# Optimization experiments

Measured on AMD Instinct MI355X. Metric: run time of the kernel, lower is better.

The kernel has to match this reference:

```python
import jax, jax.numpy as jnp
import numpy as np

N = 100_000   # total nodes across all subgraphs in batch
E = 1_600_000 # edges (avg degree 16)
B = 1_000     # number of subgraphs
D = 128       # in_dim = out_dim
SZ = N // B   # nodes per subgraph


def setup_inputs() -> dict:
    key = jax.random.key(0)
    ks = jax.random.split(key, 8)
    feat = jax.random.normal(ks[0], (N, D), dtype=jnp.float32)
    edge_src = jax.random.randint(ks[1], (E,), 0, N, dtype=jnp.int32)
    edge_dst = jax.random.randint(ks[2], (E,), 0, N, dtype=jnp.int32)
    # pre-normalized edge weights (is_normed=True path)
    edge_w = jax.random.uniform(ks[3], (E,), dtype=jnp.float32)
    s = 1.0 / np.sqrt(D)
    W1 = jax.random.normal(ks[4], (D, D), dtype=jnp.float32) * s
    W2 = jax.random.normal(ks[5], (D, D), dtype=jnp.float32) * s
    Wp = jax.random.normal(ks[6], (D, D), dtype=jnp.float32) * s
    b1 = jnp.zeros((D,), jnp.float32)
    b2 = jnp.zeros((D,), jnp.float32)
    bp = jnp.zeros((D,), jnp.float32)
    # contiguous equal-size subgraphs; target = first node of each subgraph
    seg_ids = jnp.repeat(jnp.arange(B, dtype=jnp.int32), SZ)
    target = jnp.arange(B, dtype=jnp.int32) * SZ
    size_subg = jnp.full((B,), float(SZ), jnp.float32)
    return dict(feat=feat, edge_w=edge_w, W1=W1, b1=b1, W2=W2, b2=b2,
                Wp=Wp, bp=bp, size_subg=size_subg,
                edge_src=edge_src, edge_dst=edge_dst,
                seg_ids=seg_ids, target=target)


def _gcn_layer(x, src, dst, w, W, b):
    # sparse A_hat @ x : gather src features, weight, scatter-add into dst
    msg = x[src] * w[:, None]                       # [E, D]
    agg = jax.ops.segment_sum(msg, dst, num_segments=N)  # [N, D]
    return jax.nn.relu(agg @ W + b)


def reference(feat, edge_w, W1, b1, W2, b2, Wp, bp, size_subg,
              edge_src, edge_dst, seg_ids, target):
    # two stacked GCN layers (self.structure = [structure1, structure2])
    h1 = _gcn_layer(feat, edge_src, edge_dst, edge_w, W1, b1)
    h2 = _gcn_layer(h1, edge_src, edge_dst, edge_w, W2, b2)
    # ResPool: residual-sum over layer outputs, mean pool per subgraph,
    # add target-node embedding (residual), then linear + relu
    h = h1 + h2                                              # [N, D]
    pooled = jax.ops.segment_sum(h, seg_ids, num_segments=B)
    pooled = pooled / size_subg[:, None] + h[target]         # [B, D]
    emb = jax.nn.relu(pooled @ Wp + bp)
    # F.normalize(p=2, dim=1), eps=1e-12
    norm = jnp.sqrt(jnp.sum(emb * emb, axis=1, keepdims=True))
    emb = emb / jnp.maximum(norm, 1e-12)
    return emb  # EnsembleDummy just returns the single branch
```

## Files before the change

### kernel.cpp

```cpp
#include <hip/hip_runtime.h>

#define DD 128
#define CHUNK 4096
#define BSH 8
#define MAXBK 512
#define MAXCH 512
#define CAP 6144
#define CAPN 48
#define SLDS 4608

typedef _Float16 half8 __attribute__((ext_vector_type(8)));
typedef _Float16 half4v __attribute__((ext_vector_type(4)));
typedef float floatx4 __attribute__((ext_vector_type(4)));
typedef float floatx2 __attribute__((ext_vector_type(2)));

__global__ __launch_bounds__(512) void k_hist(const int* __restrict__ dst,
                                              int* __restrict__ histT, int E) {
    __shared__ int lhist[MAXBK];
    int tid = threadIdx.x;
    lhist[tid] = 0;
    __syncthreads();
    int beg = blockIdx.x * CHUNK;
    int end = min(beg + CHUNK, E);
    for (int k = beg + tid; k < end; k += 512)
        atomicAdd(&lhist[dst[k] >> BSH], 1);
    __syncthreads();
    histT[tid * MAXCH + blockIdx.x] = lhist[tid];
}

__global__ __launch_bounds__(512) void k_scanprep(int* __restrict__ histT,
                                                  int* __restrict__ gcur, int nChunks,
                                                  int NB,
                                                  const float* __restrict__ W1,
                                                  _Float16* __restrict__ W1t,
                                                  const float* __restrict__ W2,
                                                  _Float16* __restrict__ W2t) {
    if (blockIdx.x < NB) {
        __shared__ int wsum[8];
        int b = blockIdx.x;
        int c = threadIdx.x;
        int v = (c < nChunks) ? histT[b * MAXCH + c] : 0;
        int lane = c & 63, wave = c >> 6;
        int inc = v;
        #pragma unroll
        for (int off = 1; off < 64; off <<= 1) {
            int t = __shfl_up(inc, off, 64);
            if (lane >= off) inc += t;
        }
        if (lane == 63) wsum[wave] = inc;
        __syncthreads();
        if (c == 0) {
            int run = 0;
            #pragma unroll
            for (int j = 0; j < 8; ++j) { int t = wsum[j]; wsum[j] = run; run += t; }
        }
        __syncthreads();
        int ex = inc - v + wsum[wave];
        if (c < nChunks) histT[b * MAXCH + c] = ex;
        if (c == nChunks - 1) gcur[b] = ex + v;
    } else {
        int idx = (blockIdx.x - NB) * 512 + threadIdx.x;
        if (idx < 2 * DD * DD) {
            const float* W = (idx < DD * DD) ? W1 : W2;
            _Float16* Wt = (idx < DD * DD) ? W1t : W2t;
            int id = idx & (DD * DD - 1);
            int n = id >> 7, k = id & 127;
            Wt[n * DD + k] = (_Float16)W[k * DD + n];
        }
    }
}

__global__ __launch_bounds__(512) void k_pass1(const int* __restrict__ src,
                                               const int* __restrict__ dst,
                                               const float* __restrict__ w,
                                               const int* __restrict__ histT,
                                               int2* __restrict__ out, int E, int NB) {
    __shared__ int2 stg[CHUNK];
    __shared__ unsigned short bok[CHUNK];
    __shared__ int lhist[MAXBK];
    __shared__ int loff[MAXBK];
    __shared__ int lbase[MAXBK];
    __shared__ int lcur[MAXBK];
    int tid = threadIdx.x;
    lhist[tid] = 0;
    __syncthreads();

    int beg = blockIdx.x * CHUNK;
    int end = min(beg + CHUNK, E);
    for (int k = beg + tid; k < end; k += 512)
        atomicAdd(&lhist[dst[k] >> BSH], 1);
    __syncthreads();
    if (tid < 64) {
        int base = tid * 8, v[8], s = 0;
        #pragma unroll
        for (int j = 0; j < 8; ++j) { v[j] = lhist[base + j]; s += v[j]; }
        int scn = s;
        #pragma unroll
        for (int off = 1; off < 64; off <<= 1) {
            int t = __shfl_up(scn, off, 64);
            if (tid >= off) scn += t;
        }
        int ex = scn - s;
        #pragma unroll
        for (int j = 0; j < 8; ++j) { loff[base + j] = ex; lcur[base + j] = ex; ex += v[j]; }
    }
    __syncthreads();
    if (tid < NB)
        lbase[tid] = tid * CAP + histT[tid * MAXCH + blockIdx.x];
    for (int k = beg + tid; k < end; k += 512) {
        int d = dst[k];
        int b = d >> BSH;
        int p = atomicAdd(&lcur[b], 1);
        stg[p] = make_int2(src[k] | ((d & ((1 << BSH) - 1)) << 17),
                           __float_as_int(w[k]));
        bok[p] = (unsigned short)b;
    }
    __syncthreads();
    int total = end - beg;
    for (int j = tid; j < total; j += 512) {
        int b = bok[j];
        out[lbase[b] + (j - loff[b])] = stg[j];
    }
}

__global__ __launch_bounds__(512) void k_p2g1(const int2* __restrict__ bkt,
                                              const int* __restrict__ gcur,
                                              int* __restrict__ cnt,
                                              int2* __restrict__ edges, int N, int NB,
                                              const float* __restrict__ A,
                                              const _Float16* __restrict__ Wt,
                                              unsigned char* __restrict__ Y, int nrows) {
    if (blockIdx.x < NB) {
        __shared__ int2 stg[SLDS];
        __shared__ int lhist[1 << BSH];
        __shared__ int loff[1 << BSH];
        __shared__ int lcur[1 << BSH];
        int tid = threadIdx.x;
        int b = blockIdx.x;
        int base = b * CAP;
        int nrec = gcur[b];
        int nl = min(nrec, SLDS);
        int d0 = b << BSH;

        if (tid < (1 << BSH)) lhist[tid] = 0;
        for (int i = tid; i < nl; i += 512)
            stg[i] = bkt[base + i];
        __syncthreads();
        for (int i = tid; i < nl; i += 512)
            atomicAdd(&lhist[(unsigned)stg[i].x >> 17], 1);
        for (int i = SLDS + tid; i < nrec; i += 512)
            atomicAdd(&lhist[(unsigned)bkt[base + i].x >> 17], 1);
        __syncthreads();
        if (tid < 64) {
            int bs = tid * 4, vv[4], s = 0;
            #pragma unroll
            for (int j = 0; j < 4; ++j) { vv[j] = lhist[bs + j]; s += vv[j]; }
            int scn = s;
            #pragma unroll
            for (int off = 1; off < 64; off <<= 1) {
                int t = __shfl_up(scn, off, 64);
                if (tid >= off) scn += t;
            }
            int ex = scn - s;
            #pragma unroll
            for (int j = 0; j < 4; ++j) {
                loff[bs + j] = ex; lcur[bs + j] = ex; ex += vv[j];
            }
        }
        __syncthreads();
        if (tid < (1 << BSH)) {
            int d = d0 + tid;
            if (d < N)
                cnt[d] = min(lhist[tid], CAPN);
        }
        for (int i = tid; i < nl; i += 512) {
            int2 r = stg[i];
            int dl = (unsigned)r.x >> 17;
            int slot = atomicAdd(&lcur[dl], 1) - loff[dl];
            if (slot < CAPN)
                edges[(size_t)(d0 + dl) * CAPN + slot] = make_int2(r.x & 0x1FFFF, r.y);
        }
        for (int i = SLDS + tid; i < nrec; i += 512) {
            int2 r = bkt[base + i];
            int dl = (unsigned)r.x >> 17;
            int slot = atomicAdd(&lcur[dl], 1) - loff[dl];
            if (slot < CAPN)
                edges[(size_t)(d0 + dl) * CAPN + slot] = make_int2(r.x & 0x1FFFF, r.y);
        }
    } else {
        int gblk = blockIdx.x - NB;
        int wave = threadIdx.x >> 6;
        int lane = threadIdx.x & 63;
        int row0 = gblk * 256 + wave * 32;
        int m = lane & 15;
        int q = lane >> 4;
        int r0 = min(row0 + m, nrows - 1);
        int r1 = min(row0 + 16 + m, nrows - 1);

        floatx4 acc[2][8];
        #pragma unroll
        for (int t = 0; t < 2; ++t)
            #pragma unroll
            for (int c = 0; c < 8; ++c)
                acc[t][c] = (floatx4){0.f, 0.f, 0.f, 0.f};

        #pragma unroll
        for (int ks = 0; ks < 4; ++ks) {
            int kbase = ks * 32 + q * 8;
            float4 x0 = *reinterpret_cast<const float4*>(A + (size_t)r0 * DD + kbase);
            float4 x1 = *reinterpret_cast<const float4*>(A + (size_t)r0 * DD + kbase + 4);
            float4 y0 = *reinterpret_cast<const float4*>(A + (size_t)r1 * DD + kbase);
            float4 y1 = *reinterpret_cast<const float4*>(A + (size_t)r1 * DD + kbase + 4);
            half8 a0, a1;
            a0[0]=(_Float16)x0.x; a0[1]=(_Float16)x0.y; a0[2]=(_Float16)x0.z; a0[3]=(_Float16)x0.w;
            a0[4]=(_Float16)x1.x; a0[5]=(_Float16)x1.y; a0[6]=(_Float16)x1.z; a0[7]=(_Float16)x1.w;
            a1[0]=(_Float16)y0.x; a1[1]=(_Float16)y0.y; a1[2]=(_Float16)y0.z; a1[3]=(_Float16)y0.w;
            a1[4]=(_Float16)y1.x; a1[5]=(_Float16)y1.y; a1[6]=(_Float16)y1.z; a1[7]=(_Float16)y1.w;
            #pragma unroll
            for (int c = 0; c < 8; ++c) {
                half8 b = *reinterpret_cast<const half8*>(Wt + (size_t)(c * 16 + m) * DD + kbase);
                acc[0][c] = __builtin_amdgcn_mfma_f32_16x16x32_f16(b, a0, acc[0][c], 0, 0, 0);
                acc[1][c] = __builtin_amdgcn_mfma_f32_16x16x32_f16(b, a1, acc[1][c], 0, 0, 0);
            }
        }

        #pragma unroll
        for (int t = 0; t < 2; ++t) {
            int row = row0 + t * 16 + m;
            if (row >= nrows) continue;
            size_t rb = (size_t)row * DD;
            #pragma unroll
            for (int c = 0; c < 8; ++c) {
                int col = c * 16 + q * 4;
                int u = 0;
                u = __builtin_amdgcn_cvt_pk_fp8_f32(acc[t][c][0], acc[t][c][1], u, false);
                u = __builtin_amdgcn_cvt_pk_fp8_f32(acc[t][c][2], acc[t][c][3], u, true);
                *reinterpret_cast<unsigned int*>(&Y[rb + col]) = (unsigned int)u;
            }
        }
    }
}

__global__ __launch_bounds__(256) void k_gemm_f16A(const _Float16* __restrict__ A,
                                                   const _Float16* __restrict__ Wt,
                                                   unsigned char* __restrict__ Y,
                                                   int nrows) {
    int wave = threadIdx.x >> 6;
    int lane = threadIdx.x & 63;
    int row0 = blockIdx.x * 128 + wave * 32;
    int m = lane & 15;
    int q = lane >> 4;

    floatx4 acc[2][8];
    #pragma unroll
    for (int t = 0; t < 2; ++t)
        #pragma unroll
        for (int c = 0; c < 8; ++c)
            acc[t][c] = (floatx4){0.f, 0.f, 0.f, 0.f};

    #pragma unroll
    for (int ks = 0; ks < 4; ++ks) {
        int kbase = ks * 32 + q * 8;
        half8 a0 = *reinterpret_cast<const half8*>(A + (size_t)(row0 + m) * DD + kbase);
        half8 a1 = *reinterpret_cast<const half8*>(A + (size_t)(row0 + 16 + m) * DD + kbase);
        #pragma unroll
        for (int c = 0; c < 8; ++c) {
            half8 b = *reinterpret_cast<const half8*>(Wt + (size_t)(c * 16 + m) * DD + kbase);
            acc[0][c] = __builtin_amdgcn_mfma_f32_16x16x32_f16(b, a0, acc[0][c], 0, 0, 0);
            acc[1][c] = __builtin_amdgcn_mfma_f32_16x16x32_f16(b, a1, acc[1][c], 0, 0, 0);
        }
    }

    #pragma unroll
    for (int t = 0; t < 2; ++t) {
        int row = row0 + t * 16 + m;
        if (row >= nrows) continue;
        size_t rb = (size_t)row * DD;
        #pragma unroll
        for (int c = 0; c < 8; ++c) {
            int col = c * 16 + q * 4;
            int u = 0;
            u = __builtin_amdgcn_cvt_pk_fp8_f32(acc[t][c][0], acc[t][c][1], u, false);
            u = __builtin_amdgcn_cvt_pk_fp8_f32(acc[t][c][2], acc[t][c][3], u, true);
            *reinterpret_cast<unsigned int*>(&Y[rb + col]) = (unsigned int)u;
        }
    }
}

__global__ __launch_bounds__(256) void k_agg_eplg(const unsigned char* __restrict__ x,
                                                  const int* __restrict__ cnt,
                                                  const int2* __restrict__ edges,
                                                  const float* __restrict__ bias,
                                                  const _Float16* __restrict__ resid,
                                                  _Float16* __restrict__ out, int N) {
    int gwave = (blockIdx.x * blockDim.x + threadIdx.x) >> 6;
    int lane = threadIdx.x & 63;
    int half = lane >> 5;
    int hl = lane & 31;
    int wid = gwave * 2 + half;
    if (wid >= N) return;
    int g = hl >> 3;
    int sl = hl & 7;
    int c = cnt[wid];
    int beg = wid * CAPN;
    floatx2 acc2[8];
    #pragma unroll
    for (int j = 0; j < 8; ++j) acc2[j] = (floatx2){0.f, 0.f};

    int2 e[8];
    #pragma unroll
    for (int u = 0; u < 8; ++u) e[u] = edges[beg + u * 4 + g];
    uint4 v[8];
    #pragma unroll
    for (int u = 0; u < 8; ++u) {
        int row = min(max(e[u].x, 0), N - 1);
        v[u] = *reinterpret_cast<const uint4*>(x + (size_t)row * DD + sl * 16);
    }
    int end = min(c, CAPN);
    #pragma unroll
    for (int u = 0; u < 8; ++u) {
        float wv = (u * 4 + g < end) ? __int_as_float(e[u].y) : 0.f;
        floatx2 w2 = (floatx2){wv, wv};
        acc2[0] += __builtin_amdgcn_cvt_pk_f32_fp8((int)v[u].x, false) * w2;
        acc2[1] += __builtin_amdgcn_cvt_pk_f32_fp8((int)v[u].x, true)  * w2;
        acc2[2] += __builtin_amdgcn_cvt_pk_f32_fp8((int)v[u].y, false) * w2;
        acc2[3] += __builtin_amdgcn_cvt_pk_f32_fp8((int)v[u].y, true)  * w2;
        acc2[4] += __builtin_amdgcn_cvt_pk_f32_fp8((int)v[u].z, false) * w2;
        acc2[5] += __builtin_amdgcn_cvt_pk_f32_fp8((int)v[u].z, true)  * w2;
        acc2[6] += __builtin_amdgcn_cvt_pk_f32_fp8((int)v[u].w, false) * w2;
        acc2[7] += __builtin_amdgcn_cvt_pk_f32_fp8((int)v[u].w, true)  * w2;
    }
    if (end > 32) {
        int2 e2[4];
        #pragma unroll
        for (int u = 0; u < 4; ++u) e2[u] = edges[beg + 32 + u * 4 + g];
        uint4 v2[4];
        #pragma unroll
        for (int u = 0; u < 4; ++u) {
            int row = min(max(e2[u].x, 0), N - 1);
            v2[u] = *reinterpret_cast<const uint4*>(x + (size_t)row * DD + sl * 16);
        }
        #pragma unroll
        for (int u = 0; u < 4; ++u) {
            float wv = (32 + u * 4 + g < end) ? __int_as_float(e2[u].y) : 0.f;
            floatx2 w2 = (floatx2){wv, wv};
            acc2[0] += __builtin_amdgcn_cvt_pk_f32_fp8((int)v2[u].x, false) * w2;
            acc2[1] += __builtin_amdgcn_cvt_pk_f32_fp8((int)v2[u].x, true)  * w2;
            acc2[2] += __builtin_amdgcn_cvt_pk_f32_fp8((int)v2[u].y, false) * w2;
            acc2[3] += __builtin_amdgcn_cvt_pk_f32_fp8((int)v2[u].y, true)  * w2;
            acc2[4] += __builtin_amdgcn_cvt_pk_f32_fp8((int)v2[u].z, false) * w2;
            acc2[5] += __builtin_amdgcn_cvt_pk_f32_fp8((int)v2[u].z, true)  * w2;
            acc2[6] += __builtin_amdgcn_cvt_pk_f32_fp8((int)v2[u].w, false) * w2;
            acc2[7] += __builtin_amdgcn_cvt_pk_f32_fp8((int)v2[u].w, true)  * w2;
        }
    }

    #pragma unroll
    for (int j = 0; j < 8; ++j) {
        acc2[j][0] += __shfl_xor(acc2[j][0], 8, 64);
        acc2[j][1] += __shfl_xor(acc2[j][1], 8, 64);
        acc2[j][0] += __shfl_xor(acc2[j][0], 16, 64);
        acc2[j][1] += __shfl_xor(acc2[j][1], 16, 64);
    }
    if (g == 0) {
        float acc[16];
        #pragma unroll
        for (int j = 0; j < 8; ++j) { acc[2 * j] = acc2[j][0]; acc[2 * j + 1] = acc2[j][1]; }
        size_t rb = (size_t)wid * DD + sl * 16;
        float bb[16];
        #pragma unroll
        for (int q = 0; q < 4; ++q) {
            float4 b4 = *reinterpret_cast<const float4*>(&bias[sl * 16 + q * 4]);
            bb[q * 4 + 0] = b4.x; bb[q * 4 + 1] = b4.y;
            bb[q * 4 + 2] = b4.z; bb[q * 4 + 3] = b4.w;
        }
        half8 o0, o1;
        if (resid) {
            half8 r0 = *reinterpret_cast<const half8*>(&resid[rb]);
            half8 r1 = *reinterpret_cast<const half8*>(&resid[rb + 8]);
            #pragma unroll
            for (int j = 0; j < 8; ++j) {
                float v = acc[j] + bb[j];
                v = v > 0.f ? v : 0.f;
                o0[j] = (_Float16)(v + (float)r0[j]);
            }
            #pragma unroll
            for (int j = 0; j < 8; ++j) {
                float v = acc[8 + j] + bb[8 + j];
                v = v > 0.f ? v : 0.f;
                o1[j] = (_Float16)(v + (float)r1[j]);
            }
        } else {
            #pragma unroll
            for (int j = 0; j < 8; ++j) {
                float v = acc[j] + bb[j];
                o0[j] = (_Float16)(v > 0.f ? v : 0.f);
            }
            #pragma unroll
            for (int j = 0; j < 8; ++j) {
                float v = acc[8 + j] + bb[8 + j];
                o1[j] = (_Float16)(v > 0.f ? v : 0.f);
            }
        }
        *reinterpret_cast<half8*>(&out[rb]) = o0;
        *reinterpret_cast<half8*>(&out[rb + 8]) = o1;
    }
}

__global__ __launch_bounds__(256) void k_pool_final(const _Float16* __restrict__ h,
                                                    const int* __restrict__ target,
                                                    const float* __restrict__ size_subg,
                                                    const float* __restrict__ Wp,
                                                    const float* __restrict__ bp,
                                                    float* __restrict__ out, int SZ) {
    __shared__ float part[16][DD];
    __shared__ float p[DD];
    __shared__ float wsum[2];
    int b = blockIdx.x;
    int t = threadIdx.x;
    int c = t & 15;
    int r = t >> 4;
    const _Float16* hp = h + (size_t)b * SZ * DD;
    float s[8] = {0.f, 0.f, 0.f, 0.f, 0.f, 0.f, 0.f, 0.f};
    for (int n = r; n < SZ; n += 16) {
        half8 v = *reinterpret_cast<const half8*>(hp + (size_t)n * DD + c * 8);
        #pragma unroll
        for (int j = 0; j < 8; ++j) s[j] += (float)v[j];
    }
    #pragma unroll
    for (int j = 0; j < 8; ++j) part[r][c * 8 + j] = s[j];
    __syncthreads();
    if (t < DD) {
        float sum = 0.f;
        #pragma unroll
        for (int rr = 0; rr < 16; ++rr) sum += part[rr][t];
        int tg = target[b];
        p[t] = sum / size_subg[b] + (float)h[(size_t)tg * DD + t];
    }
    __syncthreads();
    if (t < DD) {
        float acc = 0.f;
        #pragma unroll 4
        for (int k = 0; k < DD; ++k) acc = fmaf(p[k], Wp[k * DD + t], acc);
        float e = acc + bp[t];
        e = e > 0.f ? e : 0.f;
        float sq = e * e;
        #pragma unroll
        for (int off = 32; off > 0; off >>= 1) sq += __shfl_down(sq, off, 64);
        int lane = t & 63, w = t >> 6;
        if (lane == 0) wsum[w] = sq;
        __syncthreads();
        float norm = sqrtf(wsum[0] + wsum[1]);
        float scale = 1.f / fmaxf(norm, 1e-12f);
        out[b * DD + t] = e * scale;
    } else {
        __syncthreads();
    }
}

extern "C" void kernel_launch(void* const* d_in, const int* in_sizes, int n_in,
                              void* d_out, int out_size, void* d_ws, size_t ws_size,
                              hipStream_t stream) {
    const float* feat      = (const float*)d_in[0];
    const float* edge_w    = (const float*)d_in[1];
    const float* W1        = (const float*)d_in[2];
    const float* b1        = (const float*)d_in[3];
    const float* W2        = (const float*)d_in[4];
    const float* b2        = (const float*)d_in[5];
    const float* Wp        = (const float*)d_in[6];
    const float* bp        = (const float*)d_in[7];
    const float* size_subg = (const float*)d_in[8];
    const int*   edge_src  = (const int*)d_in[9];
    const int*   edge_dst  = (const int*)d_in[10];
    const int*   target    = (const int*)d_in[12];

    const int N  = in_sizes[0] / DD;
    const int E  = in_sizes[1];
    const int B  = in_sizes[8];
    const int SZ = N / B;

    const int P  = ((N + 127) / 128) * 128;
    const int NB = (N + (1 << BSH) - 1) >> BSH;
    const int nChunks = (E + CHUNK - 1) / CHUNK;

    char* ws = (char*)d_ws;
    size_t off = 0;
    auto alloc = [&](size_t bytes) {
        void* p = ws + off;
        off += (bytes + 255) & ~(size_t)255;
        return p;
    };
    unsigned char* Y = (unsigned char*)alloc((size_t)P * DD);
    _Float16* h1     = (_Float16*)alloc((size_t)P * DD * 2);
    _Float16* H      = (_Float16*)alloc((size_t)P * DD * 2);
    _Float16* W1t    = (_Float16*)alloc((size_t)DD * DD * 2);
    _Float16* W2t    = (_Float16*)alloc((size_t)DD * DD * 2);
    int*   cnt       = (int*)alloc((size_t)N * 4);
    int*   gcur      = (int*)alloc((size_t)MAXBK * 4);
    int*   histT     = (int*)alloc((size_t)MAXBK * MAXCH * 4);
    int2*  edges_bkt = (int2*)alloc((size_t)NB * CAP * 8);
    int2*  edges     = (int2*)alloc((size_t)N * CAPN * 8);

    k_hist<<<nChunks, 512, 0, stream>>>(edge_dst, histT, E);

    int prepBlocks = (2 * DD * DD + 511) / 512;
    k_scanprep<<<NB + prepBlocks, 512, 0, stream>>>(histT, gcur, nChunks, NB,
                                                    W1, W1t, W2, W2t);

    k_pass1<<<nChunks, 512, 0, stream>>>(edge_src, edge_dst, edge_w, histT,
                                         edges_bkt, E, NB);

    int g1Blocks = (N + 255) / 256;
    k_p2g1<<<NB + g1Blocks, 512, 0, stream>>>(edges_bkt, gcur, cnt, edges, N, NB,
                                              feat, W1t, Y, N);

    int nodePairs  = (N + 1) / 2;
    int aggBlocks  = (nodePairs * 64 + 255) / 256;
    int gemmBlocks = (N + 127) / 128;

    k_agg_eplg<<<aggBlocks, 256, 0, stream>>>(Y, cnt, edges, b1, nullptr, h1, N);
    k_gemm_f16A<<<gemmBlocks, 256, 0, stream>>>(h1, W2t, Y, N);
    k_agg_eplg<<<aggBlocks, 256, 0, stream>>>(Y, cnt, edges, b2, h1, H, N);
    k_pool_final<<<B, 256, 0, stream>>>(H, target, size_subg, Wp, bp,
                                        (float*)d_out, SZ);
}
```

Measured before the change: 297.5 us.

## Merge four binning/prep kernels into one cooperative persistent kernel with grid syncs

Replaces the separate histogram, scan/weight-prep, pass1 scatter and pass2+GEMM1 kernels with a single cooperative-launch persistent kernel that separates phases with grid.sync(). The intent is to remove kernel launch gaps and tail effects between the small preprocessing stages. The chunk size is halved to create more work items, and the scan now handles two chunks per thread. The cost is grid-wide barrier overhead, a grid capped at occupancy times 256 CUs, and the GEMM phase now runs with 512-thread persistent blocks looping over items.

Result: slower. 445.9 us (+49.9%).

```diff
diff --git a/kernel.cpp b/kernel.cpp
--- a/kernel.cpp
+++ b/kernel.cpp
@@ -1,241 +1,259 @@
 #include <hip/hip_runtime.h>
+#include <hip/hip_cooperative_groups.h>
+
+namespace cg = cooperative_groups;
 
 #define DD 128
-#define CHUNK 4096
+#define CHUNK 2048
 #define BSH 8
 #define MAXBK 512
-#define MAXCH 512
+#define MAXCH 1024
 #define CAP 6144
 #define CAPN 48
 #define SLDS 4608
+#define SMEMB 40960
 
 typedef _Float16 half8 __attribute__((ext_vector_type(8)));
-typedef _Float16 half4v __attribute__((ext_vector_type(4)));
 typedef float floatx4 __attribute__((ext_vector_type(4)));
 typedef float floatx2 __attribute__((ext_vector_type(2)));
 
-__global__ __launch_bounds__(512) void k_hist(const int* __restrict__ dst,
-                                              int* __restrict__ histT, int E) {
-    __shared__ int lhist[MAXBK];
+extern "C" __global__ void __launch_bounds__(512, 1)
+k_bin_coop(const int* __restrict__ src, const int* __restrict__ dst,
+           const float* __restrict__ w,
+           int* __restrict__ histT, int* __restrict__ gcur, int* __restrict__ cnt,
+           int2* __restrict__ edges_bkt, int2* __restrict__ edges,
+           int E, int N, int NB, int nChunks,
+           const float* __restrict__ W1, _Float16* __restrict__ W1t,
+           const float* __restrict__ W2, _Float16* __restrict__ W2t,
+           const float* __restrict__ A, unsigned char* __restrict__ Y,
+           int nrows, int g1Blocks) {
+    __shared__ __align__(16) char smem[SMEMB];
+    cg::grid_group grid = cg::this_grid();
     int tid = threadIdx.x;
-    lhist[tid] = 0;
-    __syncthreads();
-    int beg = blockIdx.x * CHUNK;
-    int end = min(beg + CHUNK, E);
-    for (int k = beg + tid; k < end; k += 512)
-        atomicAdd(&lhist[dst[k] >> BSH], 1);
-    __syncthreads();
-    histT[tid * MAXCH + blockIdx.x] = lhist[tid];
-}
-
-__global__ __launch_bounds__(512) void k_scanprep(int* __restrict__ histT,
-                                                  int* __restrict__ gcur, int nChunks,
-                                                  int NB,
-                                                  const float* __restrict__ W1,
-                                                  _Float16* __restrict__ W1t,
-                                                  const float* __restrict__ W2,
-                                                  _Float16* __restrict__ W2t) {
-    if (blockIdx.x < NB) {
-        __shared__ int wsum[8];
-        int b = blockIdx.x;
-        int c = threadIdx.x;
-        int v = (c < nChunks) ? histT[b * MAXCH + c] : 0;
-        int lane = c & 63, wave = c >> 6;
-        int inc = v;
-        #pragma unroll
-        for (int off = 1; off < 64; off <<= 1) {
-            int t = __shfl_up(inc, off, 64);
-            if (lane >= off) inc += t;
-        }
-        if (lane == 63) wsum[wave] = inc;
-        __syncthreads();
-        if (c == 0) {
-            int run = 0;
-            #pragma unroll
-            for (int j = 0; j < 8; ++j) { int t = wsum[j]; wsum[j] = run; run += t; }
-        }
-        __syncthreads();
-        int ex = inc - v + wsum[wave];
-        if (c < nChunks) histT[b * MAXCH + c] = ex;
-        if (c == nChunks - 1) gcur[b] = ex + v;
-    } else {
-        int idx = (blockIdx.x - NB) * 512 + threadIdx.x;
-        if (idx < 2 * DD * DD) {
-            const float* W = (idx < DD * DD) ? W1 : W2;
-            _Float16* Wt = (idx < DD * DD) ? W1t : W2t;
-            int id = idx & (DD * DD - 1);
-            int n = id >> 7, k = id & 127;
-            Wt[n * DD + k] = (_Float16)W[k * DD + n];
-        }
-    }
-}
-
-__global__ __launch_bounds__(512) void k_pass1(const int* __restrict__ src,
-                                               const int* __restrict__ dst,
-                                               const float* __restrict__ w,
-                                               const int* __restrict__ histT,
-                                               int2* __restrict__ out, int E, int NB) {
-    __shared__ int2 stg[CHUNK];
-    __shared__ unsigned short bok[CHUNK];
-    __shared__ int lhist[MAXBK];
-    __shared__ int loff[MAXBK];
-    __shared__ int lbase[MAXBK];
-    __shared__ int lcur[MAXBK];
-    int tid = threadIdx.x;
-    lhist[tid] = 0;
-    __syncthreads();
-
-    int beg = blockIdx.x * CHUNK;
-    int end = min(beg + CHUNK, E);
-    for (int k = beg + tid; k < end; k += 512)
-        atomicAdd(&lhist[dst[k] >> BSH], 1);
-    __syncthreads();
-    if (tid < 64) {
-        int base = tid * 8, v[8], s = 0;
-        #pragma unroll
-        for (int j = 0; j < 8; ++j) { v[j] = lhist[base + j]; s += v[j]; }
-        int scn = s;
-        #pragma unroll
-        for (int off = 1; off < 64; off <<= 1) {
-            int t = __shfl_up(scn, off, 64);
-            if (tid >= off) scn += t;
-        }
-        int ex = scn - s;
-        #pragma unroll
-        for (int j = 0; j < 8; ++j) { loff[base + j] = ex; lcur[base + j] = ex; ex += v[j]; }
-    }
-    __syncthreads();
-    if (tid < NB)
-        lbase[tid] = tid * CAP + histT[tid * MAXCH + blockIdx.x];
-    for (int k = beg + tid; k < end; k += 512) {
-        int d = dst[k];
-        int b = d >> BSH;
-        int p = atomicAdd(&lcur[b], 1);
-        stg[p] = make_int2(src[k] | ((d & ((1 << BSH) - 1)) << 17),
-                           __float_as_int(w[k]));
-        bok[p] = (unsigned short)b;
-    }
-    __syncthreads();
-    int total = end - beg;
-    for (int j = tid; j < total; j += 512) {
-        int b = bok[j];
-        out[lbase[b] + (j - loff[b])] = stg[j];
-    }
-}
-
-__global__ __launch_bounds__(512) void k_p2g1(const int2* __restrict__ bkt,
-                                              const int* __restrict__ gcur,
-                                              int* __restrict__ cnt,
-                                              int2* __restrict__ edges, int N, int NB,
-                                              const float* __restrict__ A,
-                                              const _Float16* __restrict__ Wt,
-                                              unsigned char* __restrict__ Y, int nrows) {
-    if (blockIdx.x < NB) {
-        __shared__ int2 stg[SLDS];
-        __shared__ int lhist[1 << BSH];
-        __shared__ int loff[1 << BSH];
-        __shared__ int lcur[1 << BSH];
-        int tid = threadIdx.x;
-        int b = blockIdx.x;
-        int base = b * CAP;
-        int nrec = gcur[b];
-        int nl = min(nrec, SLDS);
-        int d0 = b << BSH;
-
-        if (tid < (1 << BSH)) lhist[tid] = 0;
-        for (int i = tid; i < nl; i += 512)
-            stg[i] = bkt[base + i];
-        __syncthreads();
-        for (int i = tid; i < nl; i += 512)
-            atomicAdd(&lhist[(unsigned)stg[i].x >> 17], 1);
-        for (int i = SLDS + tid; i < nrec; i += 512)
-            atomicAdd(&lhist[(unsigned)bkt[base + i].x >> 17], 1);
-        __syncthreads();
-        if (tid < 64) {
-            int bs = tid * 4, vv[4], s = 0;
-            #pragma unroll
-            for (int j = 0; j < 4; ++j) { vv[j] = lhist[bs + j]; s += vv[j]; }
-            int scn = s;
+
+    {
+        int prepItems = (2 * DD * DD + 511) / 512;
+        for (int item = blockIdx.x; item < nChunks + prepItems; item += gridDim.x) {
+            if (item < nChunks) {
+                int* lhist = (int*)smem;
+                lhist[tid] = 0;
+                __syncthreads();
+                int beg = item * CHUNK;
+                int end = min(beg + CHUNK, E);
+                for (int k = beg + tid; k < end; k += 512)
+                    atomicAdd(&lhist[dst[k] >> BSH], 1);
+                __syncthreads();
+                histT[tid * MAXCH + item] = lhist[tid];
+                __syncthreads();
+            } else {
+                int idx = (item - nChunks) * 512 + tid;
+                if (idx < 2 * DD * DD) {
+                    const float* W = (idx < DD * DD) ? W1 : W2;
+                    _Float16* Wt = (idx < DD * DD) ? W1t : W2t;
+                    int id = idx & (DD * DD - 1);
+                    int n = id >> 7, k = id & 127;
+                    Wt[n * DD + k] = (_Float16)W[k * DD + n];
+                }
+            }
+        }
+    }
+    grid.sync();
+
+    {
+        int* wsum = (int*)smem;
+        for (int b = blockIdx.x; b < NB; b += gridDim.x) {
+            int c = tid;
+            int c0 = 2 * c, c1 = 2 * c + 1;
+            int v0 = (c0 < nChunks) ? histT[b * MAXCH + c0] : 0;
+            int v1 = (c1 < nChunks) ? histT[b * MAXCH + c1] : 0;
+            int s = v0 + v1;
+            int lane = c & 63, wave = c >> 6;
+            int inc = s;
             #pragma unroll
             for (int off = 1; off < 64; off <<= 1) {
-                int t = __shfl_up(scn, off, 64);
-                if (tid >= off) scn += t;
-            }
-            int ex = scn - s;
-            #pragma unroll
-            for (int j = 0; j < 4; ++j) {
-                loff[bs + j] = ex; lcur[bs + j] = ex; ex += vv[j];
-            }
-        }
-        __syncthreads();
-        if (tid < (1 << BSH)) {
-            int d = d0 + tid;
-            if (d < N)
-                cnt[d] = min(lhist[tid], CAPN);
-        }
-        for (int i = tid; i < nl; i += 512) {
-            int2 r = stg[i];
-            int dl = (unsigned)r.x >> 17;
-            int slot = atomicAdd(&lcur[dl], 1) - loff[dl];
-            if (slot < CAPN)
-                edges[(size_t)(d0 + dl) * CAPN + slot] = make_int2(r.x & 0x1FFFF, r.y);
-        }
-        for (int i = SLDS + tid; i < nrec; i += 512) {
-            int2 r = bkt[base + i];
-            int dl = (unsigned)r.x >> 17;
-            int slot = atomicAdd(&lcur[dl], 1) - loff[dl];
-            if (slot < CAPN)
-                edges[(size_t)(d0 + dl) * CAPN + slot] = make_int2(r.x & 0x1FFFF, r.y);
-        }
-    } else {
-        int gblk = blockIdx.x - NB;
-        int wave = threadIdx.x >> 6;
-        int lane = threadIdx.x & 63;
-        int row0 = gblk * 256 + wave * 32;
-        int m = lane & 15;
-        int q = lane >> 4;
-        int r0 = min(row0 + m, nrows - 1);
-        int r1 = min(row0 + 16 + m, nrows - 1);
-
-        floatx4 acc[2][8];
-        #pragma unroll
-        for (int t = 0; t < 2; ++t)
-            #pragma unroll
-            for (int c = 0; c < 8; ++c)
-                acc[t][c] = (floatx4){0.f, 0.f, 0.f, 0.f};
-
-        #pragma unroll
-        for (int ks = 0; ks < 4; ++ks) {
-            int kbase = ks * 32 + q * 8;
-            float4 x0 = *reinterpret_cast<const float4*>(A + (size_t)r0 * DD + kbase);
-            float4 x1 = *reinterpret_cast<const float4*>(A + (size_t)r0 * DD + kbase + 4);
-            float4 y0 = *reinterpret_cast<const float4*>(A + (size_t)r1 * DD + kbase);
-            float4 y1 = *reinterpret_cast<const float4*>(A + (size_t)r1 * DD + kbase + 4);
-            half8 a0, a1;
-            a0[0]=(_Float16)x0.x; a0[1]=(_Float16)x0.y; a0[2]=(_Float16)x0.z; a0[3]=(_Float16)x0.w;
-            a0[4]=(_Float16)x1.x; a0[5]=(_Float16)x1.y; a0[6]=(_Float16)x1.z; a0[7]=(_Float16)x1.w;
-            a1[0]=(_Float16)y0.x; a1[1]=(_Float16)y0.y; a1[2]=(_Float16)y0.z; a1[3]=(_Float16)y0.w;
-            a1[4]=(_Float16)y1.x; a1[5]=(_Float16)y1.y; a1[6]=(_Float16)y1.z; a1[7]=(_Float16)y1.w;
-            #pragma unroll
-            for (int c = 0; c < 8; ++c) {
-                half8 b = *reinterpret_cast<const half8*>(Wt + (size_t)(c * 16 + m) * DD + kbase);
-                acc[0][c] = __builtin_amdgcn_mfma_f32_16x16x32_f16(b, a0, acc[0][c], 0, 0, 0);
-                acc[1][c] = __builtin_amdgcn_mfma_f32_16x16x32_f16(b, a1, acc[1][c], 0, 0, 0);
-            }
-        }
-
-        #pragma unroll
-        for (int t = 0; t < 2; ++t) {
-            int row = row0 + t * 16 + m;
-            if (row >= nrows) continue;
-            size_t rb = (size_t)row * DD;
-            #pragma unroll
-            for (int c = 0; c < 8; ++c) {
-                int col = c * 16 + q * 4;
-                int u = 0;
-                u = __builtin_amdgcn_cvt_pk_fp8_f32(acc[t][c][0], acc[t][c][1], u, false);
-                u = __builtin_amdgcn_cvt_pk_fp8_f32(acc[t][c][2], acc[t][c][3], u, true);
-                *reinterpret_cast<unsigned int*>(&Y[rb + col]) = (unsigned int)u;
+                int t = __shfl_up(inc, off, 64);
+                if (lane >= off) inc += t;
+            }
+            if (lane == 63) wsum[wave] = inc;
+            __syncthreads();
+            if (c == 0) {
+                int run = 0;
+                #pragma unroll
+                for (int j = 0; j < 8; ++j) { int t = wsum[j]; wsum[j] = run; run += t; }
+            }
+            __syncthreads();
+            int ex = inc - s + wsum[wave];
+            if (c0 < nChunks) histT[b * MAXCH + c0] = ex;
+            if (c1 < nChunks) histT[b * MAXCH + c1] = ex + v0;
+            if (c0 < nChunks && c1 >= nChunks - 1)
+                gcur[b] = ex + v0 + v1;
+            __syncthreads();
+        }
+    }
+    grid.sync();
+
+    {
+        int2* stg = (int2*)smem;
+        unsigned short* bok = (unsigned short*)(smem + 16384);
+        int* lhist = (int*)(smem + 20480);
+        int* loff  = (int*)(smem + 22528);
+        int* lbase = (int*)(smem + 24576);
+        int* lcur  = (int*)(smem + 26624);
+        for (int item = blockIdx.x; item < nChunks; item += gridDim.x) {
+            lhist[tid] = 0;
+            __syncthreads();
+            int beg = item * CHUNK;
+            int end = min(beg + CHUNK, E);
+            for (int k = beg + tid; k < end; k += 512)
+                atomicAdd(&lhist[dst[k] >> BSH], 1);
+            __syncthreads();
+            if (tid < 64) {
+                int base = tid * 8, v[8], s = 0;
+                #pragma unroll
+                for (int j = 0; j < 8; ++j) { v[j] = lhist[base + j]; s += v[j]; }
+                int scn = s;
+                #pragma unroll
+                for (int off = 1; off < 64; off <<= 1) {
+                    int t = __shfl_up(scn, off, 64);
+                    if (tid >= off) scn += t;
+                }
+                int ex = scn - s;
+                #pragma unroll
+                for (int j = 0; j < 8; ++j) { loff[base + j] = ex; lcur[base + j] = ex; ex += v[j]; }
+            }
+            __syncthreads();
+            if (tid < NB)
+                lbase[tid] = tid * CAP + histT[tid * MAXCH + item];
+            for (int k = beg + tid; k < end; k += 512) {
+                int d = dst[k];
+                int b = d >> BSH;
+                int p = atomicAdd(&lcur[b], 1);
+                stg[p] = make_int2(src[k] | ((d & ((1 << BSH) - 1)) << 17),
+                                   __float_as_int(w[k]));
+                bok[p] = (unsigned short)b;
+            }
+            __syncthreads();
+            int total = end - beg;
+            for (int j = tid; j < total; j += 512) {
+                int b = bok[j];
+                edges_bkt[lbase[b] + (j - loff[b])] = stg[j];
+            }
+            __syncthreads();
+        }
+    }
+    grid.sync();
+
+    {
+        for (int item = blockIdx.x; item < NB + g1Blocks; item += gridDim.x) {
+            if (item < NB) {
+                int2* stg = (int2*)smem;
+                int* lhist = (int*)(smem + 36864);
+                int* loff  = (int*)(smem + 37888);
+                int* lcur  = (int*)(smem + 38912);
+                int b = item;
+                int base = b * CAP;
+                int nrec = gcur[b];
+                int nl = min(nrec, SLDS);
+                int d0 = b << BSH;
+
+                if (tid < (1 << BSH)) lhist[tid] = 0;
+                for (int i = tid; i < nl; i += 512)
+                    stg[i] = edges_bkt[base + i];
+                __syncthreads();
+                for (int i = tid; i < nl; i += 512)
+                    atomicAdd(&lhist[(unsigned)stg[i].x >> 17], 1);
+                for (int i = SLDS + tid; i < nrec; i += 512)
+                    atomicAdd(&lhist[(unsigned)edges_bkt[base + i].x >> 17], 1);
+                __syncthreads();
+                if (tid < 64) {
+                    int bs = tid * 4, vv[4], s = 0;
+                    #pragma unroll
+                    for (int j = 0; j < 4; ++j) { vv[j] = lhist[bs + j]; s += vv[j]; }
+                    int scn = s;
+                    #pragma unroll
+                    for (int off = 1; off < 64; off <<= 1) {
+                        int t = __shfl_up(scn, off, 64);
+                        if (tid >= off) scn += t;
+                    }
+                    int ex = scn - s;
+                    #pragma unroll
+                    for (int j = 0; j < 4; ++j) {
+                        loff[bs + j] = ex; lcur[bs + j] = ex; ex += vv[j];
+                    }
+                }
+                __syncthreads();
+                if (tid < (1 << BSH)) {
+                    int d = d0 + tid;
+                    if (d < N)
+                        cnt[d] = min(lhist[tid], CAPN);
+                }
+                for (int i = tid; i < nl; i += 512) {
+                    int2 r = stg[i];
+                    int dl = (unsigned)r.x >> 17;
+                    int slot = atomicAdd(&lcur[dl], 1) - loff[dl];
+                    if (slot < CAPN)
+                        edges[(size_t)(d0 + dl) * CAPN + slot] = make_int2(r.x & 0x1FFFF, r.y);
+                }
+                for (int i = SLDS + tid; i < nrec; i += 512) {
+                    int2 r = edges_bkt[base + i];
+                    int dl = (unsigned)r.x >> 17;
+                    int slot = atomicAdd(&lcur[dl], 1) - loff[dl];
+                    if (slot < CAPN)
+                        edges[(size_t)(d0 + dl) * CAPN + slot] = make_int2(r.x & 0x1FFFF, r.y);
+                }
+                __syncthreads();
+            } else {
+                int gblk = item - NB;
+                int wave = tid >> 6;
+                int lane = tid & 63;
+                int row0 = gblk * 256 + wave * 32;
+                int m = lane & 15;
+                int q = lane >> 4;
+                int r0 = min(row0 + m, nrows - 1);
+                int r1 = min(row0 + 16 + m, nrows - 1);
+
+                floatx4 acc[2][8];
+                #pragma unroll
+                for (int t = 0; t < 2; ++t)
+                    #pragma unroll
+                    for (int c = 0; c < 8; ++c)
+                        acc[t][c] = (floatx4){0.f, 0.f, 0.f, 0.f};
+
+                #pragma unroll
+                for (int ks = 0; ks < 4; ++ks) {
+                    int kbase = ks * 32 + q * 8;
+                    float4 x0 = *reinterpret_cast<const float4*>(A + (size_t)r0 * DD + kbase);
+                    float4 x1 = *reinterpret_cast<const float4*>(A + (size_t)r0 * DD + kbase + 4);
+                    float4 y0 = *reinterpret_cast<const float4*>(A + (size_t)r1 * DD + kbase);
+                    float4 y1 = *reinterpret_cast<const float4*>(A + (size_t)r1 * DD + kbase + 4);
+                    half8 a0, a1;
+                    a0[0]=(_Float16)x0.x; a0[1]=(_Float16)x0.y; a0[2]=(_Float16)x0.z; a0[3]=(_Float16)x0.w;
+                    a0[4]=(_Float16)x1.x; a0[5]=(_Float16)x1.y; a0[6]=(_Float16)x1.z; a0[7]=(_Float16)x1.w;
+                    a1[0]=(_Float16)y0.x; a1[1]=(_Float16)y0.y; a1[2]=(_Float16)y0.z; a1[3]=(_Float16)y0.w;
+                    a1[4]=(_Float16)y1.x; a1[5]=(_Float16)y1.y; a1[6]=(_Float16)y1.z; a1[7]=(_Float16)y1.w;
+                    #pragma unroll
+                    for (int c = 0; c < 8; ++c) {
+                        half8 b = *reinterpret_cast<const half8*>(W1t + (size_t)(c * 16 + m) * DD + kbase);
+                        acc[0][c] = __builtin_amdgcn_mfma_f32_16x16x32_f16(b, a0, acc[0][c], 0, 0, 0);
+                        acc[1][c] = __builtin_amdgcn_mfma_f32_16x16x32_f16(b, a1, acc[1][c], 0, 0, 0);
+                    }
+                }
+
+                #pragma unroll
+                for (int t = 0; t < 2; ++t) {
+                    int row = row0 + t * 16 + m;
+                    if (row >= nrows) continue;
+                    size_t rb = (size_t)row * DD;
+                    #pragma unroll
+                    for (int c = 0; c < 8; ++c) {
+                        int col = c * 16 + q * 4;
+                        int u = 0;
+                        u = __builtin_amdgcn_cvt_pk_fp8_f32(acc[t][c][0], acc[t][c][1], u, false);
+                        u = __builtin_amdgcn_cvt_pk_fp8_f32(acc[t][c][2], acc[t][c][3], u, true);
+                        *reinterpret_cast<unsigned int*>(&Y[rb + col]) = (unsigned int)u;
+                    }
+                }
+                __syncthreads();
             }
         }
     }
@@ -501,18 +519,30 @@
     int2*  edges_bkt = (int2*)alloc((size_t)NB * CAP * 8);
     int2*  edges     = (int2*)alloc((size_t)N * CAPN * 8);
 
-    k_hist<<<nChunks, 512, 0, stream>>>(edge_dst, histT, E);
-
-    int prepBlocks = (2 * DD * DD + 511) / 512;
-    k_scanprep<<<NB + prepBlocks, 512, 0, stream>>>(histT, gcur, nChunks, NB,
-                                                    W1, W1t, W2, W2t);
-
-    k_pass1<<<nChunks, 512, 0, stream>>>(edge_src, edge_dst, edge_w, histT,
-                                         edges_bkt, E, NB);
-
     int g1Blocks = (N + 255) / 256;
-    k_p2g1<<<NB + g1Blocks, 512, 0, stream>>>(edges_bkt, gcur, cnt, edges, N, NB,
-                                              feat, W1t, Y, N);
+    int nrowsv = N;
+
+    int prepItems = (2 * DD * DD + 511) / 512;
+    int coopItems = nChunks + prepItems;
+    if (NB + g1Blocks > coopItems) coopItems = NB + g1Blocks;
+    int maxBlkPerCU = 0;
+    (void)hipOccupancyMaxActiveBlocksPerMultiprocessor(
+        &maxBlkPerCU, reinterpret_cast<const void*>(&k_bin_coop), 512, 0);
+    if (maxBlkPerCU < 1) maxBlkPerCU = 1;
+    int coopGrid = maxBlkPerCU * 256;
+    if (coopGrid > coopItems) coopGrid = coopItems;
+
+    int Ev = E, Nv = N, NBv = NB, nCv = nChunks, g1v = g1Blocks;
+    void* kargs[] = {
+        (void*)&edge_src, (void*)&edge_dst, (void*)&edge_w,
+        (void*)&histT, (void*)&gcur, (void*)&cnt,
+        (void*)&edges_bkt, (void*)&edges,
+        (void*)&Ev, (void*)&Nv, (void*)&NBv, (void*)&nCv,
+        (void*)&W1, (void*)&W1t, (void*)&W2, (void*)&W2t,
+        (void*)&feat, (void*)&Y, (void*)&nrowsv, (void*)&g1v
+    };
+    hipLaunchCooperativeKernel(reinterpret_cast<const void*>(&k_bin_coop),
+                               dim3(coopGrid), dim3(512), kargs, 0, stream);
 
     int nodePairs  = (N + 1) / 2;
     int aggBlocks  = (nodePairs * 64 + 255) / 256;
```
